# Kernel tuning notes

Hardware: AMD Instinct MI355X
Metric: run time of the kernel (lower is better)

The kernel has to match this reference:

```python
import jax, jax.numpy as jnp
import numpy as np

D = 4096

def setup_inputs() -> dict:
    key = jax.random.key(0)
    ks = jax.random.split(key, 6)
    scale = 1.0 / np.sqrt(D)
    x = jax.random.normal(ks[0], (2, 2048, D), dtype=jnp.float32)
    W1 = jax.random.normal(ks[1], (D, D), dtype=jnp.float32) * scale
    W2 = jax.random.normal(ks[2], (D, D), dtype=jnp.float32) * scale
    W3 = jax.random.normal(ks[3], (D, D), dtype=jnp.float32) * scale
    W4 = jax.random.normal(ks[4], (D, D), dtype=jnp.float32) * scale
    W5 = jax.random.normal(ks[5], (D, D), dtype=jnp.float32) * scale
    return {"x": x, "W1": W1, "W2": W2, "W3": W3, "W4": W4, "W5": W5}

def reference(x, W1, W2, W3, W4, W5):
    # torch nn.Linear(no bias): y = x @ W.T
    xA = jnp.einsum('bsd,ed->bse', x, W1)
    xB = jnp.einsum('bsd,ed->bse', x, W2)
    xC = jnp.einsum('bsd,ed->bse', x, W3)
    # Gram over channels: [B, D, D]
    xSq = jnp.einsum('bsd,bse->bde', xA, xB)
    xSq = jax.nn.softmax(xSq, axis=-1)
    xO = jnp.einsum('bsd,bde->bse', xC, xSq)
    xO = jax.nn.softmax(xO, axis=-1)
    xO = jnp.einsum('bsd,ed->bse', xO, W4)
    xO = jax.nn.silu(xO)
    out = jnp.einsum('bsd,ed->bse', x + xO, W5)
    return out
```

## Files before the change

### kernel.cpp

```cpp
#include <hip/hip_runtime.h>
#include <hip/hip_bf16.h>
#include <type_traits>

#define DD 4096
#define SS 2048
#define BB 2

typedef float f32x4 __attribute__((ext_vector_type(4)));
typedef short bf16x8 __attribute__((ext_vector_type(8)));
typedef int i32x4 __attribute__((ext_vector_type(4)));

#define SX 21.166666f
#define SW 1354.6667f
#define SP 127.0f
#define DQ_G1 7.381890e-4f
#define DQ_GRAM 2.2320e-3f
#define DQ_G3 3.720001e-4f
#define DQ_G4 5.81252e-6f

__device__ __forceinline__ unsigned short f2b(float f) {
  unsigned int u = __float_as_uint(f);
  u += 0x7fffu + ((u >> 16) & 1u);
  return (unsigned short)(u >> 16);
}
__device__ __forceinline__ float b2f(unsigned short h) {
  return __uint_as_float((unsigned int)h << 16);
}

__device__ __forceinline__ void gll16(const char* g, char* l) {
  __builtin_amdgcn_global_load_lds(
      (const __attribute__((address_space(1))) unsigned int*)g,
      (__attribute__((address_space(3))) unsigned int*)l, 16, 0, 0);
}

#define MEMFENCE asm volatile("" ::: "memory")

#define STAGE_Q(XBASE, KT, KS, LQ)                                             \
  {                                                                            \
    gll16((XBASE) + (size_t)(wid * 16 + srow) * KB + (KT) * 128 + (KS) * 64 +  \
              scolB,                                                           \
          (char*)(LQ) + wid * 1024);                                           \
    gll16((XBASE) + (size_t)(128 + wid * 16 + srow) * KB + (KT) * 128 +        \
              (KS) * 64 + scolB,                                               \
          (char*)(LQ) + 8192 + wid * 1024);                                    \
  }

#define DO_MFMA(Cv_, Av_, Bv_)                                                 \
  if constexpr (DT == 0) {                                                     \
    Cv_ = __builtin_amdgcn_mfma_f32_16x16x32_bf16(                             \
        __builtin_bit_cast(bf16x8, Av_), __builtin_bit_cast(bf16x8, Bv_),      \
        Cv_, 0, 0, 0);                                                         \
  } else {                                                                     \
    asm("v_mfma_i32_16x16x64_i8 %0, %1, %2, %0" : "+v"(Cv_)                    \
        : "v"(Av_), "v"(Bv_));                                                 \
  }

#define PHASE(MG, KS, STAGE_STMT, TAIL_STMT)                                   \
  {                                                                            \
    if ((MG) == 0) {                                                           \
      _Pragma("unroll") for (int n_ = 0; n_ < 4; ++n_)                         \
          bq[n_] = *(const i32x4*)(slot + 32768 + (KS)*16384 +                 \
                                   (wn * 4 + n_) * 1024 + fro);                \
    }                                                                          \
    _Pragma("unroll") for (int i_ = 0; i_ < 4; ++i_)                           \
        aq[i_] = *(const i32x4*)(slot + (KS)*16384 +                           \
                                 (wm * 8 + (MG)*4 + i_) * 1024 + fro);         \
    STAGE_STMT;                                                                \
    MEMFENCE;                                                                  \
    __builtin_amdgcn_s_barrier();                                              \
    MEMFENCE;                                                                  \
    __builtin_amdgcn_s_setprio(1);                                             \
    _Pragma("unroll") for (int i_ = 0; i_ < 4; ++i_)                           \
      _Pragma("unroll") for (int n_ = 0; n_ < 4; ++n_) {                       \
        DO_MFMA(acc[(MG)*4 + i_][n_], aq[i_], bq[n_]);                         \
      }                                                                        \
    __builtin_amdgcn_s_setprio(0);                                             \
    TAIL_STMT;                                                                 \
    MEMFENCE;                                                                  \
    __builtin_amdgcn_s_barrier();                                              \
    MEMFENCE;                                                                  \
  }

template <int DT, int EPI>
__global__ __launch_bounds__(512, 2)
void gemm256(const char* __restrict__ A,
             const char* __restrict__ B,
             void* __restrict__ Cv,
             const float* __restrict__ R,
             int GM, int GN,
             int N, int KB,
             long long sAb, long long sBb, long long sCe, float dq) {
  extern __shared__ __align__(16) char lds[];
  const int tid = threadIdx.x;
  const int lane = tid & 63;
  const int wid = tid >> 6;
  const int wm = wid >> 2;
  const int wn = wid & 3;

  const int nwg = gridDim.x;
  const int cpx = nwg >> 3;
  const int wg = ((int)blockIdx.x & 7) * cpx + ((int)blockIdx.x >> 3);
  const int bz = wg / (GM * GN);
  const int rem = wg - bz * (GM * GN);
  const int bm = rem / GN;
  const int bn = rem - bm * GN;

  const char* Ab_ = A + (size_t)bz * sAb + (size_t)bm * 256 * KB;
  const char* Bb_ = B + (size_t)bz * sBb + (size_t)bn * 256 * KB;

  const int lsw = lane ^ (((lane >> 5) & 1) << 1);
  const int srow = lsw >> 2;
  const int scolB = (lsw & 3) * 16;
  const int r16 = lane & 15;
  const int c16 = ((lane >> 4) * 16) ^ ((r16 & 8) << 2);
  const int fro = r16 * 64 + c16;

  using accT = typename std::conditional<DT == 0, f32x4, i32x4>::type;
  accT acc[8][4] = {};
  i32x4 aq[4], bq[4];
  const int NK = KB >> 7;

  STAGE_Q(Ab_, 0, 0, lds + 0);
  STAGE_Q(Ab_, 0, 1, lds + 16384);
  STAGE_Q(Bb_, 0, 0, lds + 32768);
  STAGE_Q(Bb_, 0, 1, lds + 49152);
  STAGE_Q(Ab_, 1, 0, lds + 65536);
  STAGE_Q(Bb_, 1, 0, lds + 65536 + 32768);
  asm volatile("s_waitcnt vmcnt(4)" ::: "memory");
  __builtin_amdgcn_s_barrier();
  MEMFENCE;

  for (int U = 0; U < NK; ++U) {
    char* slot = lds + (U & 1) * 65536;
    char* oslot = lds + ((U & 1) ^ 1) * 65536;
    const bool g1 = (U + 1 < NK), g2 = (U + 2 < NK);
    PHASE(0, 0, { if (g1) STAGE_Q(Ab_, U + 1, 1, oslot + 16384); }, {});
    PHASE(1, 0, { if (g1) STAGE_Q(Bb_, U + 1, 1, oslot + 49152); }, {});
    PHASE(0, 1, { if (g2) STAGE_Q(Ab_, U + 2, 0, slot + 0); }, {});
    PHASE(1, 1, { if (g2) STAGE_Q(Bb_, U + 2, 0, slot + 32768); },
          {
            if (g2) { asm volatile("s_waitcnt vmcnt(4)" ::: "memory"); }
            else if (g1) { asm volatile("s_waitcnt vmcnt(0)" ::: "memory"); }
          });
  }

  const int row0 = bm * 256 + wm * 128 + (lane >> 4) * 4;
  const int col0 = bn * 256 + wn * 64 + (lane & 15);

#pragma unroll
  for (int m = 0; m < 8; ++m)
#pragma unroll
    for (int j = 0; j < 4; ++j) {
      size_t ro = (size_t)(row0 + m * 16 + j) * N;
#pragma unroll
      for (int n = 0; n < 4; ++n) {
        size_t idx = ro + col0 + n * 16;
        float v;
        if constexpr (DT == 0) v = acc[m][n][j];
        else v = (float)acc[m][n][j] * dq;
        if constexpr (DT == 0 && EPI == 1) {
          ((float*)Cv + (size_t)bz * sCe)[idx] = v;
        } else if constexpr (DT == 0 && EPI == 2) {
          float s = v / (1.f + __expf(-v));
          ((unsigned short*)Cv + (size_t)bz * sCe)[idx] = f2b(R[idx] + s);
        } else if constexpr (DT == 1 && EPI == 0) {
          float q = fminf(fmaxf(v * SX, -127.f), 127.f);
          ((char*)Cv + (size_t)bz * sCe)[idx] = (char)__float2int_rn(q);
        } else if constexpr (DT == 1 && EPI == 1) {
          ((unsigned short*)Cv + (size_t)bz * sCe)[idx] = f2b(v);
        } else if constexpr (DT == 1 && EPI == 2) {
          ((float*)Cv + (size_t)bz * sCe)[idx] = v;
        } else {
          float s = v / (1.f + __expf(-v));
          ((unsigned short*)Cv + (size_t)bz * sCe)[idx] = f2b(R[idx] + s);
        }
      }
    }
}

__device__ __forceinline__ float wred_max(float v) {
#pragma unroll
  for (int o = 32; o > 0; o >>= 1) v = fmaxf(v, __shfl_xor(v, o, 64));
  return v;
}
__device__ __forceinline__ float wred_sum(float v) {
#pragma unroll
  for (int o = 32; o > 0; o >>= 1) v += __shfl_xor(v, o, 64);
  return v;
}

__global__ __launch_bounds__(256)
void row_stats_bf16(const unsigned short* __restrict__ X, float* __restrict__ smax,
                    float* __restrict__ ssum) {
  const size_t row = blockIdx.x;
  const uint4* p = (const uint4*)(X + row * DD);
  const int t = threadIdx.x;
  uint4 u[2];
  u[0] = p[t];
  u[1] = p[t + 256];
  float fv[16];
#pragma unroll
  for (int q = 0; q < 2; ++q) {
    const unsigned int* w = (const unsigned int*)&u[q];
#pragma unroll
    for (int j = 0; j < 4; ++j) {
      fv[q * 8 + j * 2 + 0] = b2f((unsigned short)(w[j] & 0xFFFFu));
      fv[q * 8 + j * 2 + 1] = b2f((unsigned short)(w[j] >> 16));
    }
  }
  float m = -1e30f;
#pragma unroll
  for (int i = 0; i < 16; ++i) m = fmaxf(m, fv[i]);
  __shared__ float rb[8];
  float wm = wred_max(m);
  if ((t & 63) == 0) rb[t >> 6] = wm;
  __syncthreads();
  const float gm = fmaxf(fmaxf(rb[0], rb[1]), fmaxf(rb[2], rb[3]));
  float s = 0.f;
#pragma unroll
  for (int i = 0; i < 16; ++i) s += __expf(fv[i] - gm);
  float wsum = wred_sum(s);
  if ((t & 63) == 0) rb[4 + (t >> 6)] = wsum;
  __syncthreads();
  if (t == 0) { smax[row] = gm; ssum[row] = rb[4] + rb[5] + rb[6] + rb[7]; }
}

__global__ __launch_bounds__(256)
void exp_transpose_i8(const unsigned short* __restrict__ X,
                      const float* __restrict__ smax,
                      const float* __restrict__ ssum,
                      char* __restrict__ PT) {
  const int b = blockIdx.z;
  const int d0 = blockIdx.y * 64;
  const int e0 = blockIdx.x * 64;
  __shared__ char lt[64][68];
  const int t = threadIdx.x;
  const int tr = t >> 4;
  const int tc = (t & 15) * 4;
  const unsigned short* Xb = X + (size_t)b * DD * DD;
#pragma unroll
  for (int rr = 0; rr < 64; rr += 16) {
    const int dd = rr + tr;
    ushort4 v = *(const ushort4*)&Xb[(size_t)(d0 + dd) * DD + e0 + tc];
    const float mx = smax[(size_t)b * DD + d0 + dd];
    const float inv = 127.f / ssum[(size_t)b * DD + d0 + dd];
    lt[dd][tc + 0] = (char)__float2int_rn(__expf(b2f(v.x) - mx) * inv);
    lt[dd][tc + 1] = (char)__float2int_rn(__expf(b2f(v.y) - mx) * inv);
    lt[dd][tc + 2] = (char)__float2int_rn(__expf(b2f(v.z) - mx) * inv);
    lt[dd][tc + 3] = (char)__float2int_rn(__expf(b2f(v.w) - mx) * inv);
  }
  __syncthreads();
  char* Pb = PT + (size_t)b * DD * DD;
#pragma unroll
  for (int rr = 0; rr < 64; rr += 16) {
    const int ee = rr + tr;
    char4 o;
    o.x = lt[tc + 0][ee];
    o.y = lt[tc + 1][ee];
    o.z = lt[tc + 2][ee];
    o.w = lt[tc + 3][ee];
    *(char4*)&Pb[(size_t)(e0 + ee) * DD + d0 + tc] = o;
  }
}

__global__ __launch_bounds__(256)
void row_softmax_i8(const float* __restrict__ X, char* __restrict__ Y) {
  const size_t row = blockIdx.x;
  const float4* p = (const float4*)(X + row * DD);
  const int t = threadIdx.x;
  float4 v[4];
  float m = -1e30f;
#pragma unroll
  for (int q = 0; q < 4; ++q) {
    v[q] = p[q * 256 + t];
    m = fmaxf(m, fmaxf(fmaxf(v[q].x, v[q].y), fmaxf(v[q].z, v[q].w)));
  }
  __shared__ float rb[8];
  float wm = wred_max(m);
  if ((t & 63) == 0) rb[t >> 6] = wm;
  __syncthreads();
  const float gm = fmaxf(fmaxf(rb[0], rb[1]), fmaxf(rb[2], rb[3]));
  float s = 0.f;
#pragma unroll
  for (int q = 0; q < 4; ++q) {
    v[q].x = __expf(v[q].x - gm); v[q].y = __expf(v[q].y - gm);
    v[q].z = __expf(v[q].z - gm); v[q].w = __expf(v[q].w - gm);
    s += v[q].x + v[q].y + v[q].z + v[q].w;
  }
  float wsum = wred_sum(s);
  if ((t & 63) == 0) rb[4 + (t >> 6)] = wsum;
  __syncthreads();
  const float inv = SP / (rb[4] + rb[5] + rb[6] + rb[7]);
  char4* yo = (char4*)(Y + row * DD);
#pragma unroll
  for (int q = 0; q < 4; ++q) {
    char4 o;
    o.x = (char)__float2int_rn(fminf(v[q].x * inv, 127.f));
    o.y = (char)__float2int_rn(fminf(v[q].y * inv, 127.f));
    o.z = (char)__float2int_rn(fminf(v[q].z * inv, 127.f));
    o.w = (char)__float2int_rn(fminf(v[q].w * inv, 127.f));
    yo[q * 256 + t] = o;
  }
}

__global__ __launch_bounds__(256)
void cvt_bf16(const float* __restrict__ X, unsigned short* __restrict__ Y, size_t n4) {
  size_t i = (size_t)blockIdx.x * 256 + threadIdx.x;
  const size_t stride = (size_t)gridDim.x * 256;
  for (; i < n4; i += stride) {
    float4 v = ((const float4*)X)[i];
    ushort4 o;
    o.x = f2b(v.x); o.y = f2b(v.y); o.z = f2b(v.z); o.w = f2b(v.w);
    ((ushort4*)Y)[i] = o;
  }
}

__global__ __launch_bounds__(256)
void cvt_i8(const float* __restrict__ X, char* __restrict__ Y, float scale, size_t n4) {
  size_t i = (size_t)blockIdx.x * 256 + threadIdx.x;
  const size_t stride = (size_t)gridDim.x * 256;
  for (; i < n4; i += stride) {
    float4 v = ((const float4*)X)[i];
    char4 o;
    o.x = (char)__float2int_rn(fminf(fmaxf(v.x * scale, -127.f), 127.f));
    o.y = (char)__float2int_rn(fminf(fmaxf(v.y * scale, -127.f), 127.f));
    o.z = (char)__float2int_rn(fminf(fmaxf(v.z * scale, -127.f), 127.f));
    o.w = (char)__float2int_rn(fminf(fmaxf(v.w * scale, -127.f), 127.f));
    ((char4*)Y)[i] = o;
  }
}

__global__ void ws_sentinel(float* o, float v) { o[0] = v; }

extern "C" void kernel_launch(void* const* d_in, const int* in_sizes, int n_in,
                              void* d_out, int out_size, void* d_ws, size_t ws_size,
                              hipStream_t stream) {
  const float* x = (const float*)d_in[0];
  const float* W[5] = {(const float*)d_in[1], (const float*)d_in[2],
                       (const float*)d_in[3], (const float*)d_in[4],
                       (const float*)d_in[5]};
  float* out = (float*)d_out;
  char* ws = (char*)d_ws;

  const size_t MB = 1ull << 20;
  const size_t NEEDED = 144 * MB + 64 * 1024;
  if (ws_size < NEEDED) {
    ws_sentinel<<<1, 1, 0, stream>>>(out, (float)ws_size);
    return;
  }

  const int LDSB = 131072;
  hipFuncSetAttribute((const void*)gemm256<0, 1>, hipFuncAttributeMaxDynamicSharedMemorySize, LDSB);
  hipFuncSetAttribute((const void*)gemm256<1, 0>, hipFuncAttributeMaxDynamicSharedMemorySize, LDSB);
  hipFuncSetAttribute((const void*)gemm256<1, 1>, hipFuncAttributeMaxDynamicSharedMemorySize, LDSB);
  hipFuncSetAttribute((const void*)gemm256<1, 2>, hipFuncAttributeMaxDynamicSharedMemorySize, LDSB);
  hipFuncSetAttribute((const void*)gemm256<1, 3>, hipFuncAttributeMaxDynamicSharedMemorySize, LDSB);

  char* x_i8 = ws + 0;
  char* xosm_i8 = ws + 0;
  char* wi8 = ws + 16 * MB;
  unsigned short* wbuf = (unsigned short*)(ws + 32 * MB);
  char* xAT = ws + 64 * MB;
  char* xBT = ws + 80 * MB;
  char* PT = ws + 64 * MB;
  char* xC = ws + 96 * MB;
  unsigned short* y5 = (unsigned short*)(ws + 112 * MB);
  float* smax = (float*)(ws + 144 * MB);
  float* ssum = smax + (size_t)BB * DD;

  unsigned short* gram = (unsigned short*)d_out;
  float* xO = (float*)d_out;

  const size_t nW4 = (size_t)DD * DD / 4;
  const size_t nX4 = (size_t)BB * SS * DD / 4;

  cvt_i8<<<2048, 256, 0, stream>>>(x, x_i8, SX, nX4);

  cvt_i8<<<2048, 256, 0, stream>>>(W[0], wi8, SW, nW4);
  gemm256<1, 0><<<16 * 8 * BB, 512, LDSB, stream>>>(
      wi8, x_i8, xAT, nullptr, 16, 8, SS, DD, 0LL, (long long)SS * DD,
      (long long)DD * SS, DQ_G1);
  cvt_i8<<<2048, 256, 0, stream>>>(W[1], wi8, SW, nW4);
  gemm256<1, 0><<<16 * 8 * BB, 512, LDSB, stream>>>(
      wi8, x_i8, xBT, nullptr, 16, 8, SS, DD, 0LL, (long long)SS * DD,
      (long long)DD * SS, DQ_G1);
  cvt_i8<<<2048, 256, 0, stream>>>(W[2], wi8, SW, nW4);
  gemm256<1, 0><<<16 * 16, 512, LDSB, stream>>>(
      x_i8, wi8, xC, nullptr, 16, 16, DD, DD, 0LL, 0LL, 0LL, DQ_G1);
  gemm256<1, 1><<<16 * 16 * BB, 512, LDSB, stream>>>(
      xAT, xBT, gram, nullptr, 16, 16, DD, SS, (long long)DD * SS,
      (long long)DD * SS, (long long)DD * DD, DQ_GRAM);
  row_stats_bf16<<<BB * DD, 256, 0, stream>>>(gram, smax, ssum);
  exp_transpose_i8<<<dim3(DD / 64, DD / 64, BB), 256, 0, stream>>>(gram, smax, ssum, PT);
  gemm256<1, 2><<<8 * 16 * BB, 512, LDSB, stream>>>(
      xC, PT, xO, nullptr, 8, 16, DD, DD, (long long)SS * DD,
      (long long)DD * DD, (long long)SS * DD, DQ_G3);
  row_softmax_i8<<<BB * SS, 256, 0, stream>>>(xO, xosm_i8);
  cvt_i8<<<2048, 256, 0, stream>>>(W[3], wi8, SW, nW4);
  gemm256<1, 3><<<16 * 16, 512, LDSB, stream>>>(
      xosm_i8, wi8, y5, x, 16, 16, DD, DD, 0LL, 0LL, 0LL, DQ_G4);
  cvt_bf16<<<2048, 256, 0, stream>>>(W[4], wbuf, nW4);
  gemm256<0, 1><<<16 * 16, 512, LDSB, stream>>>(
      (const char*)y5, (const char*)wbuf, out, nullptr, 16, 16, DD, 2 * DD, 0LL,
      0LL, 0LL, 1.f);
}
```

Measured before the change: 674.7 us.

## Restructure GEMM to 4 waves with 128x128 per-wave tiles and simpler pipeline

```diff
diff --git a/kernel.cpp b/kernel.cpp
--- a/kernel.cpp
+++ b/kernel.cpp
@@ -37,12 +37,10 @@
 
 #define STAGE_Q(XBASE, KT, KS, LQ)                                             \
   {                                                                            \
-    gll16((XBASE) + (size_t)(wid * 16 + srow) * KB + (KT) * 128 + (KS) * 64 +  \
-              scolB,                                                           \
-          (char*)(LQ) + wid * 1024);                                           \
-    gll16((XBASE) + (size_t)(128 + wid * 16 + srow) * KB + (KT) * 128 +        \
-              (KS) * 64 + scolB,                                               \
-          (char*)(LQ) + 8192 + wid * 1024);                                    \
+    _Pragma("unroll") for (int q_ = 0; q_ < 4; ++q_)                           \
+        gll16((XBASE) + (size_t)(q_ * 64 + wid * 16 + srow) * KB +             \
+                  (KT) * 128 + (KS) * 64 + scolB,                              \
+              (char*)(LQ) + (q_ * 4 + wid) * 1024);                            \
   }
 
 #define DO_MFMA(Cv_, Av_, Bv_)                                                 \
@@ -51,38 +49,27 @@
         __builtin_bit_cast(bf16x8, Av_), __builtin_bit_cast(bf16x8, Bv_),      \
         Cv_, 0, 0, 0);                                                         \
   } else {                                                                     \
-    asm("v_mfma_i32_16x16x64_i8 %0, %1, %2, %0" : "+v"(Cv_)                    \
-        : "v"(Av_), "v"(Bv_));                                                 \
-  }
-
-#define PHASE(MG, KS, STAGE_STMT, TAIL_STMT)                                   \
+    Cv_ = __builtin_amdgcn_mfma_i32_16x16x64_i8(Av_, Bv_, Cv_, 0, 0, 0);       \
+  }
+
+#define KS_BLOCK(KS, STAGE_STMT, TAIL_STMT)                                    \
   {                                                                            \
-    if ((MG) == 0) {                                                           \
-      _Pragma("unroll") for (int n_ = 0; n_ < 4; ++n_)                         \
-          bq[n_] = *(const i32x4*)(slot + 32768 + (KS)*16384 +                 \
-                                   (wn * 4 + n_) * 1024 + fro);                \
-    }                                                                          \
-    _Pragma("unroll") for (int i_ = 0; i_ < 4; ++i_)                           \
-        aq[i_] = *(const i32x4*)(slot + (KS)*16384 +                           \
-                                 (wm * 8 + (MG)*4 + i_) * 1024 + fro);         \
+    _Pragma("unroll") for (int i_ = 0; i_ < 8; ++i_)                           \
+        aq[i_] = *(const i32x4*)(slot + (KS)*16384 + (wm * 8 + i_) * 1024 +    \
+                                 fro);                                         \
+    _Pragma("unroll") for (int n_ = 0; n_ < 8; ++n_)                           \
+        bq[n_] = *(const i32x4*)(slot + 32768 + (KS)*16384 +                   \
+                                 (wn * 8 + n_) * 1024 + fro);                  \
     STAGE_STMT;                                                                \
-    MEMFENCE;                                                                  \
-    __builtin_amdgcn_s_barrier();                                              \
-    MEMFENCE;                                                                  \
-    __builtin_amdgcn_s_setprio(1);                                             \
-    _Pragma("unroll") for (int i_ = 0; i_ < 4; ++i_)                           \
-      _Pragma("unroll") for (int n_ = 0; n_ < 4; ++n_) {                       \
-        DO_MFMA(acc[(MG)*4 + i_][n_], aq[i_], bq[n_]);                         \
+    _Pragma("unroll") for (int i_ = 0; i_ < 8; ++i_)                           \
+      _Pragma("unroll") for (int n_ = 0; n_ < 8; ++n_) {                       \
+        DO_MFMA(acc[i_][n_], aq[i_], bq[n_]);                                  \
       }                                                                        \
-    __builtin_amdgcn_s_setprio(0);                                             \
     TAIL_STMT;                                                                 \
-    MEMFENCE;                                                                  \
-    __builtin_amdgcn_s_barrier();                                              \
-    MEMFENCE;                                                                  \
   }
 
 template <int DT, int EPI>
-__global__ __launch_bounds__(512, 2)
+__global__ __launch_bounds__(256, 1)
 void gemm256(const char* __restrict__ A,
              const char* __restrict__ B,
              void* __restrict__ Cv,
@@ -94,8 +81,8 @@
   const int tid = threadIdx.x;
   const int lane = tid & 63;
   const int wid = tid >> 6;
-  const int wm = wid >> 2;
-  const int wn = wid & 3;
+  const int wm = wid >> 1;
+  const int wn = wid & 1;
 
   const int nwg = gridDim.x;
   const int cpx = nwg >> 3;
@@ -116,36 +103,49 @@
   const int fro = r16 * 64 + c16;
 
   using accT = typename std::conditional<DT == 0, f32x4, i32x4>::type;
-  accT acc[8][4] = {};
-  i32x4 aq[4], bq[4];
+  accT acc[8][8] = {};
+  i32x4 aq[8], bq[8];
   const int NK = KB >> 7;
 
   STAGE_Q(Ab_, 0, 0, lds + 0);
   STAGE_Q(Ab_, 0, 1, lds + 16384);
   STAGE_Q(Bb_, 0, 0, lds + 32768);
   STAGE_Q(Bb_, 0, 1, lds + 49152);
-  STAGE_Q(Ab_, 1, 0, lds + 65536);
-  STAGE_Q(Bb_, 1, 0, lds + 65536 + 32768);
-  asm volatile("s_waitcnt vmcnt(4)" ::: "memory");
+  asm volatile("s_waitcnt vmcnt(0)" ::: "memory");
   __builtin_amdgcn_s_barrier();
   MEMFENCE;
 
   for (int U = 0; U < NK; ++U) {
     char* slot = lds + (U & 1) * 65536;
     char* oslot = lds + ((U & 1) ^ 1) * 65536;
-    const bool g1 = (U + 1 < NK), g2 = (U + 2 < NK);
-    PHASE(0, 0, { if (g1) STAGE_Q(Ab_, U + 1, 1, oslot + 16384); }, {});
-    PHASE(1, 0, { if (g1) STAGE_Q(Bb_, U + 1, 1, oslot + 49152); }, {});
-    PHASE(0, 1, { if (g2) STAGE_Q(Ab_, U + 2, 0, slot + 0); }, {});
-    PHASE(1, 1, { if (g2) STAGE_Q(Bb_, U + 2, 0, slot + 32768); },
-          {
-            if (g2) { asm volatile("s_waitcnt vmcnt(4)" ::: "memory"); }
-            else if (g1) { asm volatile("s_waitcnt vmcnt(0)" ::: "memory"); }
-          });
+    const bool g1 = (U + 1 < NK);
+    KS_BLOCK(0,
+             {
+               if (g1) {
+                 STAGE_Q(Ab_, U + 1, 0, oslot + 0);
+                 STAGE_Q(Ab_, U + 1, 1, oslot + 16384);
+               }
+             },
+             {});
+    KS_BLOCK(1,
+             {
+               if (g1) {
+                 STAGE_Q(Bb_, U + 1, 0, oslot + 32768);
+                 STAGE_Q(Bb_, U + 1, 1, oslot + 49152);
+               }
+             },
+             {
+               if (g1) {
+                 asm volatile("s_waitcnt vmcnt(0)" ::: "memory");
+                 MEMFENCE;
+                 __builtin_amdgcn_s_barrier();
+                 MEMFENCE;
+               }
+             });
   }
 
   const int row0 = bm * 256 + wm * 128 + (lane >> 4) * 4;
-  const int col0 = bn * 256 + wn * 64 + (lane & 15);
+  const int col0 = bn * 256 + wn * 128 + (lane & 15);
 
 #pragma unroll
   for (int m = 0; m < 8; ++m)
@@ -153,7 +153,7 @@
     for (int j = 0; j < 4; ++j) {
       size_t ro = (size_t)(row0 + m * 16 + j) * N;
 #pragma unroll
-      for (int n = 0; n < 4; ++n) {
+      for (int n = 0; n < 8; ++n) {
         size_t idx = ro + col0 + n * 16;
         float v;
         if constexpr (DT == 0) v = acc[m][n][j];
@@ -377,30 +377,30 @@
   cvt_i8<<<2048, 256, 0, stream>>>(x, x_i8, SX, nX4);
 
   cvt_i8<<<2048, 256, 0, stream>>>(W[0], wi8, SW, nW4);
-  gemm256<1, 0><<<16 * 8 * BB, 512, LDSB, stream>>>(
+  gemm256<1, 0><<<16 * 8 * BB, 256, LDSB, stream>>>(
       wi8, x_i8, xAT, nullptr, 16, 8, SS, DD, 0LL, (long long)SS * DD,
       (long long)DD * SS, DQ_G1);
   cvt_i8<<<2048, 256, 0, stream>>>(W[1], wi8, SW, nW4);
-  gemm256<1, 0><<<16 * 8 * BB, 512, LDSB, stream>>>(
+  gemm256<1, 0><<<16 * 8 * BB, 256, LDSB, stream>>>(
       wi8, x_i8, xBT, nullptr, 16, 8, SS, DD, 0LL, (long long)SS * DD,
       (long long)DD * SS, DQ_G1);
   cvt_i8<<<2048, 256, 0, stream>>>(W[2], wi8, SW, nW4);
-  gemm256<1, 0><<<16 * 16, 512, LDSB, stream>>>(
+  gemm256<1, 0><<<16 * 16, 256, LDSB, stream>>>(
       x_i8, wi8, xC, nullptr, 16, 16, DD, DD, 0LL, 0LL, 0LL, DQ_G1);
-  gemm256<1, 1><<<16 * 16 * BB, 512, LDSB, stream>>>(
+  gemm256<1, 1><<<16 * 16 * BB, 256, LDSB, stream>>>(
       xAT, xBT, gram, nullptr, 16, 16, DD, SS, (long long)DD * SS,
       (long long)DD * SS, (long long)DD * DD, DQ_GRAM);
   row_stats_bf16<<<BB * DD, 256, 0, stream>>>(gram, smax, ssum);
   exp_transpose_i8<<<dim3(DD / 64, DD / 64, BB), 256, 0, stream>>>(gram, smax, ssum, PT);
-  gemm256<1, 2><<<8 * 16 * BB, 512, LDSB, stream>>>(
+  gemm256<1, 2><<<8 * 16 * BB, 256, LDSB, stream>>>(
       xC, PT, xO, nullptr, 8, 16, DD, DD, (long long)SS * DD,
       (long long)DD * DD, (long long)SS * DD, DQ_G3);
   row_softmax_i8<<<BB * SS, 256, 0, stream>>>(xO, xosm_i8);
   cvt_i8<<<2048, 256, 0, stream>>>(W[3], wi8, SW, nW4);
-  gemm256<1, 3><<<16 * 16, 512, LDSB, stream>>>(
+  gemm256<1, 3><<<16 * 16, 256, LDSB, stream>>>(
       xosm_i8, wi8, y5, x, 16, 16, DD, DD, 0LL, 0LL, 0LL, DQ_G4);
   cvt_bf16<<<2048, 256, 0, stream>>>(W[4], wbuf, nW4);
-  gemm256<0, 1><<<16 * 16, 512, LDSB, stream>>>(
+  gemm256<0, 1><<<16 * 16, 256, LDSB, stream>>>(
       (const char*)y5, (const char*)wbuf, out, nullptr, 16, 16, DD, 2 * DD, 0LL,
       0LL, 0LL, 1.f);
 }
```

Result: slower. 734.9 us (+8.9%).

## Batch xA/xB projections into one GEMM and store xO as bf16

Applied to the files above, without the earlier changes.

```diff
diff --git a/kernel.cpp b/kernel.cpp
--- a/kernel.cpp
+++ b/kernel.cpp
@@ -51,8 +51,7 @@
         __builtin_bit_cast(bf16x8, Av_), __builtin_bit_cast(bf16x8, Bv_),      \
         Cv_, 0, 0, 0);                                                         \
   } else {                                                                     \
-    asm("v_mfma_i32_16x16x64_i8 %0, %1, %2, %0" : "+v"(Cv_)                    \
-        : "v"(Av_), "v"(Bv_));                                                 \
+    Cv_ = __builtin_amdgcn_mfma_i32_16x16x64_i8(Av_, Bv_, Cv_, 0, 0, 0);       \
   }
 
 #define PHASE(MG, KS, STAGE_STMT, TAIL_STMT)                                   \
@@ -264,43 +263,51 @@
 }
 
 __global__ __launch_bounds__(256)
-void row_softmax_i8(const float* __restrict__ X, char* __restrict__ Y) {
+void row_softmax_i8b(const unsigned short* __restrict__ X, char* __restrict__ Y) {
   const size_t row = blockIdx.x;
-  const float4* p = (const float4*)(X + row * DD);
+  const uint4* p = (const uint4*)(X + row * DD);
   const int t = threadIdx.x;
-  float4 v[4];
+  uint4 u[2];
+  u[0] = p[t];
+  u[1] = p[t + 256];
+  float fv[16];
+#pragma unroll
+  for (int q = 0; q < 2; ++q) {
+    const unsigned int* w = (const unsigned int*)&u[q];
+#pragma unroll
+    for (int j = 0; j < 4; ++j) {
+      fv[q * 8 + j * 2 + 0] = b2f((unsigned short)(w[j] & 0xFFFFu));
+      fv[q * 8 + j * 2 + 1] = b2f((unsigned short)(w[j] >> 16));
+    }
+  }
   float m = -1e30f;
 #pragma unroll
-  for (int q = 0; q < 4; ++q) {
-    v[q] = p[q * 256 + t];
-    m = fmaxf(m, fmaxf(fmaxf(v[q].x, v[q].y), fmaxf(v[q].z, v[q].w)));
-  }
+  for (int i = 0; i < 16; ++i) m = fmaxf(m, fv[i]);
   __shared__ float rb[8];
   float wm = wred_max(m);
   if ((t & 63) == 0) rb[t >> 6] = wm;
   __syncthreads();
   const float gm = fmaxf(fmaxf(rb[0], rb[1]), fmaxf(rb[2], rb[3]));
   float s = 0.f;
-#pragma unroll
-  for (int q = 0; q < 4; ++q) {
-    v[q].x = __expf(v[q].x - gm); v[q].y = __expf(v[q].y - gm);
-    v[q].z = __expf(v[q].z - gm); v[q].w = __expf(v[q].w - gm);
-    s += v[q].x + v[q].y + v[q].z + v[q].w;
-  }
+  float ev[16];
+#pragma unroll
+  for (int i = 0; i < 16; ++i) { ev[i] = __expf(fv[i] - gm); s += ev[i]; }
   float wsum = wred_sum(s);
   if ((t & 63) == 0) rb[4 + (t >> 6)] = wsum;
   __syncthreads();
   const float inv = SP / (rb[4] + rb[5] + rb[6] + rb[7]);
-  char4* yo = (char4*)(Y + row * DD);
-#pragma unroll
-  for (int q = 0; q < 4; ++q) {
-    char4 o;
-    o.x = (char)__float2int_rn(fminf(v[q].x * inv, 127.f));
-    o.y = (char)__float2int_rn(fminf(v[q].y * inv, 127.f));
-    o.z = (char)__float2int_rn(fminf(v[q].z * inv, 127.f));
-    o.w = (char)__float2int_rn(fminf(v[q].w * inv, 127.f));
-    yo[q * 256 + t] = o;
-  }
+  unsigned long long w0 = 0, w1 = 0;
+#pragma unroll
+  for (int j = 0; j < 8; ++j) {
+    unsigned char c0 =
+        (unsigned char)(char)__float2int_rn(fminf(ev[j] * inv, 127.f));
+    unsigned char c1 =
+        (unsigned char)(char)__float2int_rn(fminf(ev[8 + j] * inv, 127.f));
+    w0 |= (unsigned long long)c0 << (8 * j);
+    w1 |= (unsigned long long)c1 << (8 * j);
+  }
+  ((unsigned long long*)(Y + row * DD))[t] = w0;
+  ((unsigned long long*)(Y + row * DD + 2048))[t] = w1;
 }
 
 __global__ __launch_bounds__(256)
@@ -353,15 +360,14 @@
   hipFuncSetAttribute((const void*)gemm256<0, 1>, hipFuncAttributeMaxDynamicSharedMemorySize, LDSB);
   hipFuncSetAttribute((const void*)gemm256<1, 0>, hipFuncAttributeMaxDynamicSharedMemorySize, LDSB);
   hipFuncSetAttribute((const void*)gemm256<1, 1>, hipFuncAttributeMaxDynamicSharedMemorySize, LDSB);
-  hipFuncSetAttribute((const void*)gemm256<1, 2>, hipFuncAttributeMaxDynamicSharedMemorySize, LDSB);
   hipFuncSetAttribute((const void*)gemm256<1, 3>, hipFuncAttributeMaxDynamicSharedMemorySize, LDSB);
 
   char* x_i8 = ws + 0;
   char* xosm_i8 = ws + 0;
+  char* w12_i8 = ws + 16 * MB;
   char* wi8 = ws + 16 * MB;
   unsigned short* wbuf = (unsigned short*)(ws + 32 * MB);
-  char* xAT = ws + 64 * MB;
-  char* xBT = ws + 80 * MB;
+  char* xAB = ws + 64 * MB;
   char* PT = ws + 64 * MB;
   char* xC = ws + 96 * MB;
   unsigned short* y5 = (unsigned short*)(ws + 112 * MB);
@@ -369,33 +375,31 @@
   float* ssum = smax + (size_t)BB * DD;
 
   unsigned short* gram = (unsigned short*)d_out;
-  float* xO = (float*)d_out;
+  unsigned short* xO = (unsigned short*)d_out;
 
   const size_t nW4 = (size_t)DD * DD / 4;
   const size_t nX4 = (size_t)BB * SS * DD / 4;
 
   cvt_i8<<<2048, 256, 0, stream>>>(x, x_i8, SX, nX4);
 
-  cvt_i8<<<2048, 256, 0, stream>>>(W[0], wi8, SW, nW4);
-  gemm256<1, 0><<<16 * 8 * BB, 512, LDSB, stream>>>(
-      wi8, x_i8, xAT, nullptr, 16, 8, SS, DD, 0LL, (long long)SS * DD,
-      (long long)DD * SS, DQ_G1);
-  cvt_i8<<<2048, 256, 0, stream>>>(W[1], wi8, SW, nW4);
-  gemm256<1, 0><<<16 * 8 * BB, 512, LDSB, stream>>>(
-      wi8, x_i8, xBT, nullptr, 16, 8, SS, DD, 0LL, (long long)SS * DD,
-      (long long)DD * SS, DQ_G1);
+  cvt_i8<<<2048, 256, 0, stream>>>(W[0], w12_i8, SW, nW4);
+  cvt_i8<<<2048, 256, 0, stream>>>(W[1], w12_i8 + 16 * MB, SW, nW4);
+  gemm256<1, 0><<<32 * 8 * BB, 512, LDSB, stream>>>(
+      w12_i8, x_i8, xAB, nullptr, 32, 8, SS, DD, 0LL, (long long)SS * DD,
+      (long long)2 * DD * SS, DQ_G1);
   cvt_i8<<<2048, 256, 0, stream>>>(W[2], wi8, SW, nW4);
   gemm256<1, 0><<<16 * 16, 512, LDSB, stream>>>(
       x_i8, wi8, xC, nullptr, 16, 16, DD, DD, 0LL, 0LL, 0LL, DQ_G1);
   gemm256<1, 1><<<16 * 16 * BB, 512, LDSB, stream>>>(
-      xAT, xBT, gram, nullptr, 16, 16, DD, SS, (long long)DD * SS,
-      (long long)DD * SS, (long long)DD * DD, DQ_GRAM);
+      xAB, xAB + (size_t)DD * SS, gram, nullptr, 16, 16, DD, SS,
+      (long long)2 * DD * SS, (long long)2 * DD * SS, (long long)DD * DD,
+      DQ_GRAM);
   row_stats_bf16<<<BB * DD, 256, 0, stream>>>(gram, smax, ssum);
   exp_transpose_i8<<<dim3(DD / 64, DD / 64, BB), 256, 0, stream>>>(gram, smax, ssum, PT);
-  gemm256<1, 2><<<8 * 16 * BB, 512, LDSB, stream>>>(
+  gemm256<1, 1><<<8 * 16 * BB, 512, LDSB, stream>>>(
       xC, PT, xO, nullptr, 8, 16, DD, DD, (long long)SS * DD,
       (long long)DD * DD, (long long)SS * DD, DQ_G3);
-  row_softmax_i8<<<BB * SS, 256, 0, stream>>>(xO, xosm_i8);
+  row_softmax_i8b<<<BB * SS, 256, 0, stream>>>(xO, xosm_i8);
   cvt_i8<<<2048, 256, 0, stream>>>(W[3], wi8, SW, nW4);
   gemm256<1, 3><<<16 * 16, 512, LDSB, stream>>>(
       xosm_i8, wi8, y5, x, 16, 16, DD, DD, 0LL, 0LL, 0LL, DQ_G4);
```

Measured after the change: 666.3 us, median of 2. About the same (-1.2%).
